# Kernel optimization log

Hardware: AMD Instinct MI355X
Metric: run time of the kernel (lower is better)

The kernel has to match this reference:

```python
import jax, jax.numpy as jnp
import numpy as np

N_NODES = 50000
N_EDGES = 800000
N_GRAPHS = 64
IN_DIM, HID, OUT = 128, 128, 16


def gcn_conv(x, src, dst, deg_inv_sqrt, W, b):
    # x: [N, Cin]; src/dst: [E+N] (self-loops appended); W: [Cin, Cout]
    h = x @ W                                   # [N, Cout]
    norm = deg_inv_sqrt[src] * deg_inv_sqrt[dst]  # [E+N]
    msg = h[src] * norm[:, None]                # gather + scale
    out = jax.ops.segment_sum(msg, dst, num_segments=N_NODES)
    return out + b


def setup_inputs() -> dict:
    key = jax.random.key(0)
    ks = jax.random.split(key, 8)
    x = jax.random.normal(ks[0], (N_NODES, IN_DIM), dtype=jnp.float32)
    edge_index = jax.random.randint(ks[1], (2, N_EDGES), 0, N_NODES, dtype=jnp.int64)
    batch = jnp.sort(jax.random.randint(ks[2], (N_NODES,), 0, N_GRAPHS, dtype=jnp.int64))
    s = 1.0 / np.sqrt(IN_DIM)
    W1 = jax.random.normal(ks[3], (IN_DIM, HID), dtype=jnp.float32) * s
    b1 = jnp.zeros((HID,), dtype=jnp.float32)
    W2 = jax.random.normal(ks[4], (HID, HID), dtype=jnp.float32) * (1.0 / np.sqrt(HID))
    b2 = jnp.zeros((HID,), dtype=jnp.float32)
    Wfc = jax.random.normal(ks[5], (HID, OUT), dtype=jnp.float32) * (1.0 / np.sqrt(HID))
    bfc = jnp.zeros((OUT,), dtype=jnp.float32)
    return {"x": x, "edge_index": edge_index, "batch": batch,
            "W1": W1, "b1": b1, "W2": W2, "b2": b2, "Wfc": Wfc, "bfc": bfc}


def reference(x, edge_index, batch, W1, b1, W2, b2, Wfc, bfc):
    self_loops = jnp.arange(N_NODES, dtype=edge_index.dtype)
    src = jnp.concatenate([edge_index[0], self_loops])  # [E+N]
    dst = jnp.concatenate([edge_index[1], self_loops])
    deg = jax.ops.segment_sum(jnp.ones_like(dst, dtype=x.dtype), dst, num_segments=N_NODES)
    deg_inv_sqrt = jnp.where(deg > 0, jax.lax.rsqrt(deg), 0.0)

    h = jax.nn.relu(gcn_conv(x, src, dst, deg_inv_sqrt, W1, b1))
    h = jax.nn.relu(gcn_conv(h, src, dst, deg_inv_sqrt, W2, b2))

    # global mean pool over graphs
    sums = jax.ops.segment_sum(h, batch, num_segments=N_GRAPHS)         # [G, HID]
    cnts = jax.ops.segment_sum(jnp.ones((N_NODES,), h.dtype), batch, num_segments=N_GRAPHS)
    pooled = sums / jnp.maximum(cnts, 1.0)[:, None]

    return pooled @ Wfc + bfc  # [G, OUT]
```

## Files before the change

kernel.cpp:

```cpp
#include <hip/hip_runtime.h>
#include <math.h>

#define N_NODES 50000
#define N_EDGES 800000
#define N_GRAPHS 64
#define DIM 128
#define OUTD 16

#define BSHIFT 8
#define BNODES 256
#define NBUCK ((N_NODES + BNODES - 1) / BNODES)
#define TILE 2048
#define RCAP 8192
#define BSLOT 4864
#define GEMMB 256
#define BIN_GRID ((N_EDGES + TILE - 1) / TILE)

typedef __attribute__((ext_vector_type(8))) short short8;
typedef __attribute__((ext_vector_type(4))) float f32x4;

static __device__ __forceinline__ unsigned short f2bf(float f) {
    unsigned u = __float_as_uint(f);
    u += 0x7fffu + ((u >> 16) & 1u);
    return (unsigned short)(u >> 16);
}
static __device__ __forceinline__ float bfl(unsigned u) {
    return __uint_as_float(u << 16);
}
static __device__ __forceinline__ float bfh(unsigned u) {
    return __uint_as_float(u & 0xffff0000u);
}

__global__ __launch_bounds__(256) void k_init(int* __restrict__ bcnt,
                                              float* __restrict__ pool,
                                              const float* __restrict__ W2,
                                              unsigned* __restrict__ W2f) {
    int tid = threadIdx.x;
    if (tid < NBUCK) bcnt[tid] = 0;
    for (int i = tid; i < N_GRAPHS * DIM; i += 256) pool[i] = 0.f;
    for (int idx = tid; idx < (DIM / 2) * DIM; idx += 256) {
        int kp = idx >> 7;
        int n  = idx & 127;
        int k  = kp * 2;
        int kstep = kp >> 4;
        int quad  = (kp >> 2) & 3;
        int jw    = kp & 3;
        int ct    = n >> 4;
        unsigned vlo = f2bf(W2[(size_t)k * DIM + n]);
        unsigned vhi = f2bf(W2[(size_t)(k + 1) * DIM + n]);
        W2f[(((kstep * 8 + ct) * 64) + quad * 16 + (n & 15)) * 4 + jw] = vlo | (vhi << 16);
    }
}

template <int BF16IN>
static __device__ __forceinline__ void gemm_body(const void* __restrict__ Av,
                                                 const float* __restrict__ Wg,
                                                 unsigned short* __restrict__ C,
                                                 int nrows,
                                                 unsigned* smemW, unsigned* smemC,
                                                 int tile0, int tstride) {
    unsigned* Wl = smemW;
    {
        int t = threadIdx.x;
        int p = t & 63;
        int kp = p * 2;
        int n0 = (t >> 6) * 32;
        int kstep = kp >> 5;
        int quad = (kp >> 3) & 3;
        int jw = (kp & 7) >> 1;
        const float* r0 = Wg + (size_t)kp * DIM;
        const float* r1 = r0 + DIM;
        int rot = (p >> 2) & 7;
#pragma unroll
        for (int i4 = 0; i4 < 8; ++i4) {
            int nb = ((i4 + rot) & 7) * 4;
            int n = n0 + nb;
            float4 lo = *(const float4*)(r0 + n);
            float4 hi = *(const float4*)(r1 + n);
            const float* lp = &lo.x;
            const float* hp = &hi.x;
#pragma unroll
            for (int ii = 0; ii < 4; ++ii) {
                int nn = n + ii;
                int ct = nn >> 4;
                int l  = quad * 16 + (nn & 15);
                unsigned vlo = f2bf(lp[ii]);
                unsigned vhi = f2bf(hp[ii]);
                Wl[(((kstep * 8 + ct) * 64) + l) * 4 + jw] = vlo | (vhi << 16);
            }
        }
    }
    __syncthreads();

    int wid  = threadIdx.x >> 6;
    int lane = threadIdx.x & 63;
    int m    = lane & 15;
    int quad = lane >> 4;
    const short8* Wf = (const short8*)Wl;
    unsigned short* cs = (unsigned short*)smemC + wid * 4352;
    const unsigned char* cb = (const unsigned char*)smemC + wid * 8704;

    int ntiles = (nrows + 127) / 128;
    for (int tile = tile0; tile < ntiles; tile += tstride) {
        int row0 = tile * 128 + wid * 32;
        if (row0 >= nrows) continue;

        int rA = row0 + m;      if (rA >= nrows) rA = nrows - 1;
        int rB = row0 + 16 + m; if (rB >= nrows) rB = nrows - 1;

        short8 af0[4], af1[4];
        if (BF16IN) {
            const unsigned short* arowA = (const unsigned short*)Av + (size_t)rA * DIM + quad * 8;
            const unsigned short* arowB = (const unsigned short*)Av + (size_t)rB * DIM + quad * 8;
#pragma unroll
            for (int ks = 0; ks < 4; ++ks) {
                af0[ks] = *(const short8*)(arowA + ks * 32);
                af1[ks] = *(const short8*)(arowB + ks * 32);
            }
        } else {
            const float* arowA = (const float*)Av + (size_t)rA * DIM + quad * 8;
            const float* arowB = (const float*)Av + (size_t)rB * DIM + quad * 8;
#pragma unroll
            for (int ks = 0; ks < 4; ++ks) {
                float4 lo = *(const float4*)(arowA + ks * 32);
                float4 hi = *(const float4*)(arowA + ks * 32 + 4);
                short8 f;
                f[0] = (short)f2bf(lo.x); f[1] = (short)f2bf(lo.y);
                f[2] = (short)f2bf(lo.z); f[3] = (short)f2bf(lo.w);
                f[4] = (short)f2bf(hi.x); f[5] = (short)f2bf(hi.y);
                f[6] = (short)f2bf(hi.z); f[7] = (short)f2bf(hi.w);
                af0[ks] = f;
                lo = *(const float4*)(arowB + ks * 32);
                hi = *(const float4*)(arowB + ks * 32 + 4);
                f[0] = (short)f2bf(lo.x); f[1] = (short)f2bf(lo.y);
                f[2] = (short)f2bf(lo.z); f[3] = (short)f2bf(lo.w);
                f[4] = (short)f2bf(hi.x); f[5] = (short)f2bf(hi.y);
                f[6] = (short)f2bf(hi.z); f[7] = (short)f2bf(hi.w);
                af1[ks] = f;
            }
        }

        f32x4 acc0[8], acc1[8];
#pragma unroll
        for (int ct = 0; ct < 8; ++ct) {
            acc0[ct] = (f32x4){0.f, 0.f, 0.f, 0.f};
            acc1[ct] = (f32x4){0.f, 0.f, 0.f, 0.f};
        }

#pragma unroll
        for (int ks = 0; ks < 4; ++ks) {
#pragma unroll
            for (int ct = 0; ct < 8; ++ct) {
                short8 bfrag = Wf[(ks * 8 + ct) * 64 + lane];
                acc0[ct] = __builtin_amdgcn_mfma_f32_16x16x32_bf16(af0[ks], bfrag, acc0[ct], 0, 0, 0);
                acc1[ct] = __builtin_amdgcn_mfma_f32_16x16x32_bf16(af1[ks], bfrag, acc1[ct], 0, 0, 0);
            }
        }

#pragma unroll
        for (int ct = 0; ct < 8; ++ct) {
#pragma unroll
            for (int reg = 0; reg < 4; ++reg) {
                cs[(quad * 4 + reg) * 136 + ct * 16 + m]      = f2bf(acc0[ct][reg]);
                cs[(16 + quad * 4 + reg) * 136 + ct * 16 + m] = f2bf(acc1[ct][reg]);
            }
        }
#pragma unroll
        for (int i = 0; i < 8; ++i) {
            int rg = i * 4 + quad;
            int r = row0 + rg;
            if (r < nrows) {
                uint4 vv = *(const uint4*)(cb + rg * 272 + m * 16);
                *((uint4*)(C + (size_t)r * DIM) + m) = vv;
            }
        }
    }
}

__global__ __launch_bounds__(256) void k_fused1(const float* __restrict__ A,
                                                const float* __restrict__ Wg,
                                                unsigned short* __restrict__ C,
                                                int nrows,
                                                const int* __restrict__ src,
                                                const int* __restrict__ dstp,
                                                int* __restrict__ bcnt,
                                                unsigned* __restrict__ bucket_arr) {
    __shared__ unsigned smemW[32768 / 4];
    __shared__ unsigned smemC[34816 / 4];
    if (blockIdx.x >= GEMMB) {
        int* cnt  = (int*)smemW;
        int* base = cnt + NBUCK;
        int tile0 = (blockIdx.x - GEMMB) * TILE;
        for (int i = threadIdx.x; i < NBUCK; i += 256) cnt[i] = 0;
        __syncthreads();
#pragma unroll
        for (int j = 0; j < TILE / 512; ++j) {
            int e = tile0 + j * 512 + threadIdx.x * 2;
            if (e < N_EDGES) {
                int2 d = *(const int2*)(dstp + e);
                atomicAdd(&cnt[d.x >> BSHIFT], 1);
                atomicAdd(&cnt[d.y >> BSHIFT], 1);
            }
        }
        __syncthreads();
        for (int i = threadIdx.x; i < NBUCK; i += 256) {
            int c = cnt[i];
            base[i] = i * BSLOT + (c ? atomicAdd(&bcnt[i], c) : 0);
            cnt[i] = 0;
        }
        __syncthreads();
#pragma unroll
        for (int j = 0; j < TILE / 512; ++j) {
            int e = tile0 + j * 512 + threadIdx.x * 2;
            if (e < N_EDGES) {
                int2 s = *(const int2*)(src + e);
                int2 d = *(const int2*)(dstp + e);
                int b0 = d.x >> BSHIFT, b1 = d.y >> BSHIFT;
                int p0 = base[b0] + atomicAdd(&cnt[b0], 1);
                bucket_arr[p0] = (unsigned)s.x | ((unsigned)(d.x & 255) << 16);
                int p1 = base[b1] + atomicAdd(&cnt[b1], 1);
                bucket_arr[p1] = (unsigned)s.y | ((unsigned)(d.y & 255) << 16);
            }
        }
        return;
    }
    gemm_body<0>(A, Wg, C, nrows, smemW, smemC, blockIdx.x, GEMMB);
}

__global__ __launch_bounds__(256) void k_binB(const unsigned* __restrict__ barr,
                                              const int* __restrict__ bcnt,
                                              int* __restrict__ row_off,
                                              float* __restrict__ dis,
                                              unsigned short* __restrict__ csr) {
    __shared__ unsigned raw[RCAP];
    __shared__ unsigned short stage[RCAP];
    __shared__ int hist[BNODES];
    __shared__ int scn[BNODES];
    __shared__ int borig[256], bscan[256];
    int tid = threadIdx.x;
    int b = blockIdx.x;
    int n0 = b << BSHIFT;

    int cv = (tid < NBUCK) ? bcnt[tid] : 0;
    borig[tid] = cv;
    bscan[tid] = cv;
    __syncthreads();
    for (int off = 1; off < 256; off <<= 1) {
        int t = (tid >= off) ? bscan[tid - off] : 0;
        __syncthreads();
        bscan[tid] += t;
        __syncthreads();
    }
    int rbase = bscan[b] - borig[b];
    int len = borig[b];
    const unsigned* bin = barr + (size_t)b * BSLOT;

    hist[tid] = 0;
    __syncthreads();
    for (int i = tid; i < len; i += 256) {
        unsigned ed = bin[i];
        if (i < RCAP) raw[i] = ed;
        atomicAdd(&hist[ed >> 16], 1);
    }
    __syncthreads();
    int v = hist[tid];
    scn[tid] = v;
    __syncthreads();
    for (int off = 1; off < 256; off <<= 1) {
        int t = (tid >= off) ? scn[tid - off] : 0;
        __syncthreads();
        scn[tid] += t;
        __syncthreads();
    }
    int excl = scn[tid] - v;
    int n = n0 + tid;
    if (n < N_NODES) {
        row_off[n] = rbase + excl;
        dis[n] = rsqrtf((float)(v + 1));
    }
    if (b == NBUCK - 1 && tid == 0) row_off[N_NODES] = N_EDGES;
    hist[tid] = excl;
    __syncthreads();
    for (int i = tid; i < len; i += 256) {
        unsigned ed = (i < RCAP) ? raw[i] : bin[i];
        int p = atomicAdd(&hist[ed >> 16], 1);
        unsigned short sv = (unsigned short)(ed & 0xffffu);
        if (p < RCAP) stage[p] = sv;
        else csr[rbase + p] = sv;
    }
    __syncthreads();
    {
        int s0 = excl, s1 = excl + v;
        for (int i = s0 + 1; i < s1; ++i) {
            unsigned short key = stage[i];
            int j = i - 1;
            while (j >= s0 && stage[j] > key) { stage[j + 1] = stage[j]; --j; }
            stage[j + 1] = key;
        }
    }
    __syncthreads();
    int lim = min(len, RCAP);
    for (int i = tid; i < lim; i += 256)
        csr[rbase + i] = stage[i];
}

template <int MODE>
__global__ __launch_bounds__(256) void k_agg(const uint4* __restrict__ Hb4,
                                             const int* __restrict__ row_off,
                                             const unsigned short* __restrict__ csr,
                                             const float* __restrict__ dis,
                                             const float* __restrict__ bias,
                                             uint4* __restrict__ out,
                                             const int* __restrict__ batch,
                                             float* __restrict__ pool,
                                             const short8* __restrict__ W2f) {
    __shared__ unsigned char smem[8768];
    int lane = threadIdx.x & 15;
    int nl   = threadIdx.x >> 4;
    int node = blockIdx.x * 16 + nl;

    float dn = dis[node];
    float wself = dn * dn;
    uint4 hp = Hb4[(size_t)node * 16 + lane];
    float a0[8], a1[8], a2[8], a3[8];
    a0[0] = wself * bfl(hp.x); a0[1] = wself * bfh(hp.x);
    a0[2] = wself * bfl(hp.y); a0[3] = wself * bfh(hp.y);
    a0[4] = wself * bfl(hp.z); a0[5] = wself * bfh(hp.z);
    a0[6] = wself * bfl(hp.w); a0[7] = wself * bfh(hp.w);
#pragma unroll
    for (int j = 0; j < 8; ++j) { a1[j] = 0.f; a2[j] = 0.f; a3[j] = 0.f; }

    int e = row_off[node], e1 = row_off[node + 1];
    for (; e + 4 <= e1; e += 4) {
        int s0 = csr[e];     int s1 = csr[e + 1];
        int s2 = csr[e + 2]; int s3 = csr[e + 3];
        uint4 g0 = Hb4[(size_t)s0 * 16 + lane];
        uint4 g1 = Hb4[(size_t)s1 * 16 + lane];
        uint4 g2 = Hb4[(size_t)s2 * 16 + lane];
        uint4 g3 = Hb4[(size_t)s3 * 16 + lane];
        float w0 = dn * dis[s0], w1 = dn * dis[s1];
        float w2 = dn * dis[s2], w3 = dn * dis[s3];
        a0[0] = fmaf(w0, bfl(g0.x), a0[0]); a0[1] = fmaf(w0, bfh(g0.x), a0[1]);
        a0[2] = fmaf(w0, bfl(g0.y), a0[2]); a0[3] = fmaf(w0, bfh(g0.y), a0[3]);
        a0[4] = fmaf(w0, bfl(g0.z), a0[4]); a0[5] = fmaf(w0, bfh(g0.z), a0[5]);
        a0[6] = fmaf(w0, bfl(g0.w), a0[6]); a0[7] = fmaf(w0, bfh(g0.w), a0[7]);
        a1[0] = fmaf(w1, bfl(g1.x), a1[0]); a1[1] = fmaf(w1, bfh(g1.x), a1[1]);
        a1[2] = fmaf(w1, bfl(g1.y), a1[2]); a1[3] = fmaf(w1, bfh(g1.y), a1[3]);
        a1[4] = fmaf(w1, bfl(g1.z), a1[4]); a1[5] = fmaf(w1, bfh(g1.z), a1[5]);
        a1[6] = fmaf(w1, bfl(g1.w), a1[6]); a1[7] = fmaf(w1, bfh(g1.w), a1[7]);
        a2[0] = fmaf(w2, bfl(g2.x), a2[0]); a2[1] = fmaf(w2, bfh(g2.x), a2[1]);
        a2[2] = fmaf(w2, bfl(g2.y), a2[2]); a2[3] = fmaf(w2, bfh(g2.y), a2[3]);
        a2[4] = fmaf(w2, bfl(g2.z), a2[4]); a2[5] = fmaf(w2, bfh(g2.z), a2[5]);
        a2[6] = fmaf(w2, bfl(g2.w), a2[6]); a2[7] = fmaf(w2, bfh(g2.w), a2[7]);
        a3[0] = fmaf(w3, bfl(g3.x), a3[0]); a3[1] = fmaf(w3, bfh(g3.x), a3[1]);
        a3[2] = fmaf(w3, bfl(g3.y), a3[2]); a3[3] = fmaf(w3, bfh(g3.y), a3[3]);
        a3[4] = fmaf(w3, bfl(g3.z), a3[4]); a3[5] = fmaf(w3, bfh(g3.z), a3[5]);
        a3[6] = fmaf(w3, bfl(g3.w), a3[6]); a3[7] = fmaf(w3, bfh(g3.w), a3[7]);
    }
    for (; e < e1; ++e) {
        int s = csr[e];
        uint4 g = Hb4[(size_t)s * 16 + lane];
        float w = dn * dis[s];
        a0[0] = fmaf(w, bfl(g.x), a0[0]); a0[1] = fmaf(w, bfh(g.x), a0[1]);
        a0[2] = fmaf(w, bfl(g.y), a0[2]); a0[3] = fmaf(w, bfh(g.y), a0[3]);
        a0[4] = fmaf(w, bfl(g.z), a0[4]); a0[5] = fmaf(w, bfh(g.z), a0[5]);
        a0[6] = fmaf(w, bfl(g.w), a0[6]); a0[7] = fmaf(w, bfh(g.w), a0[7]);
    }

    float4 b0 = ((const float4*)bias)[lane * 2];
    float4 b1v = ((const float4*)bias)[lane * 2 + 1];
    float r[8];
    r[0] = fmaxf(a0[0] + a1[0] + a2[0] + a3[0] + b0.x, 0.f);
    r[1] = fmaxf(a0[1] + a1[1] + a2[1] + a3[1] + b0.y, 0.f);
    r[2] = fmaxf(a0[2] + a1[2] + a2[2] + a3[2] + b0.z, 0.f);
    r[3] = fmaxf(a0[3] + a1[3] + a2[3] + a3[3] + b0.w, 0.f);
    r[4] = fmaxf(a0[4] + a1[4] + a2[4] + a3[4] + b1v.x, 0.f);
    r[5] = fmaxf(a0[5] + a1[5] + a2[5] + a3[5] + b1v.y, 0.f);
    r[6] = fmaxf(a0[6] + a1[6] + a2[6] + a3[6] + b1v.z, 0.f);
    r[7] = fmaxf(a0[7] + a1[7] + a2[7] + a3[7] + b1v.w, 0.f);

    if (MODE == 2) {
        unsigned short* sA = (unsigned short*)smem;
        unsigned short* sC = (unsigned short*)smem + 2176;
        uint4 av;
        av.x = (unsigned)f2bf(r[0]) | ((unsigned)f2bf(r[1]) << 16);
        av.y = (unsigned)f2bf(r[2]) | ((unsigned)f2bf(r[3]) << 16);
        av.z = (unsigned)f2bf(r[4]) | ((unsigned)f2bf(r[5]) << 16);
        av.w = (unsigned)f2bf(r[6]) | ((unsigned)f2bf(r[7]) << 16);
        *(uint4*)(sA + nl * 136 + lane * 8) = av;
        __syncthreads();

        int wid = threadIdx.x >> 6;
        int l64 = threadIdx.x & 63;
        int m   = l64 & 15;
        int q   = l64 >> 4;
        short8 af[4];
#pragma unroll
        for (int ks = 0; ks < 4; ++ks)
            af[ks] = *(const short8*)(sA + m * 136 + ks * 32 + q * 8);
        f32x4 acc[2];
        acc[0] = (f32x4){0.f, 0.f, 0.f, 0.f};
        acc[1] = (f32x4){0.f, 0.f, 0.f, 0.f};
#pragma unroll
        for (int ks = 0; ks < 4; ++ks) {
#pragma unroll
            for (int j = 0; j < 2; ++j) {
                int ct = wid * 2 + j;
                short8 bfrag = W2f[(ks * 8 + ct) * 64 + l64];
                acc[j] = __builtin_amdgcn_mfma_f32_16x16x32_bf16(af[ks], bfrag, acc[j], 0, 0, 0);
            }
        }
#pragma unroll
        for (int j = 0; j < 2; ++j) {
#pragma unroll
            for (int reg = 0; reg < 4; ++reg)
                sC[(q * 4 + reg) * 136 + (wid * 2 + j) * 16 + m] = f2bf(acc[j][reg]);
        }
        __syncthreads();
        {
            int t = threadIdx.x;
            int row = t >> 4, ch = t & 15;
            uint4 vv = *(const uint4*)((const unsigned char*)sC + row * 272 + ch * 16);
            out[(size_t)(blockIdx.x * 16 + row) * 16 + ch] = vv;
        }
    } else {
        float* sacc = (float*)smem;
        int* sg = (int*)(smem + 16 * DIM * 4);
#pragma unroll
        for (int j = 0; j < 8; ++j) sacc[nl * DIM + lane * 8 + j] = r[j];
        if (lane == 0) sg[nl] = batch[node];
        __syncthreads();
        int c = threadIdx.x;
        if (c < DIM) {
            float acc = 0.f;
            int curg = sg[0];
#pragma unroll
            for (int n2 = 0; n2 < 16; ++n2) {
                int g = sg[n2];
                if (g != curg) {
                    atomicAdd(&pool[curg * DIM + c], acc);
                    acc = 0.f; curg = g;
                }
                acc += sacc[n2 * DIM + c];
            }
            atomicAdd(&pool[curg * DIM + c], acc);
        }
    }
}

__global__ void k_fc(const float* __restrict__ pool, const int* __restrict__ batch,
                     const float* __restrict__ Wfc, const float* __restrict__ bfc,
                     float* __restrict__ out) {
    int id = blockIdx.x * blockDim.x + threadIdx.x;
    if (id >= N_GRAPHS * OUTD) return;
    int g = id >> 4, o = id & 15;
    int lo = 0, hi = N_NODES;
    while (lo < hi) { int mid = (lo + hi) >> 1; if (batch[mid] < g) lo = mid + 1; else hi = mid; }
    int l0 = lo;
    lo = 0; hi = N_NODES;
    while (lo < hi) { int mid = (lo + hi) >> 1; if (batch[mid] < g + 1) lo = mid + 1; else hi = mid; }
    int cntg = lo - l0;
    float inv = 1.0f / fmaxf((float)cntg, 1.0f);
    float acc = bfc[o];
    const float* p = pool + g * DIM;
    for (int c = 0; c < DIM; ++c)
        acc = fmaf(p[c] * inv, Wfc[c * OUTD + o], acc);
    out[id] = acc;
}


extern "C" void kernel_launch(void* const* d_in, const int* in_sizes, int n_in,
                              void* d_out, int out_size, void* d_ws, size_t ws_size,
                              hipStream_t stream) {
    const float* x    = (const float*)d_in[0];
    const int*   ei   = (const int*)d_in[1];
    const int*   batch= (const int*)d_in[2];
    const float* W1   = (const float*)d_in[3];
    const float* b1   = (const float*)d_in[4];
    const float* W2   = (const float*)d_in[5];
    const float* b2   = (const float*)d_in[6];
    const float* Wfc  = (const float*)d_in[7];
    const float* bfc  = (const float*)d_in[8];
    float* out = (float*)d_out;

    char* ws = (char*)d_ws;
    size_t off = 0;
    auto alloc = [&](size_t bytes) -> char* {
        char* p = ws + off;
        off = (off + bytes + 255) & ~(size_t)255;
        return p;
    };
    int*      bcnt     = (int*)     alloc((size_t)NBUCK * 4);
    int*      row_off  = (int*)     alloc((size_t)(N_NODES + 1) * 4);
    float*    dis      = (float*)   alloc((size_t)N_NODES * 4);
    unsigned short* csr= (unsigned short*)alloc((size_t)N_EDGES * 2);
    unsigned* barr     = (unsigned*)alloc((size_t)NBUCK * BSLOT * 4);
    float*    pool     = (float*)   alloc((size_t)N_GRAPHS * DIM * 4);
    unsigned* W2f      = (unsigned*)alloc((size_t)(DIM / 2) * DIM * 4);
    unsigned short* Hb = (unsigned short*)alloc((size_t)N_NODES * DIM * 2);
    unsigned short* Hb2= (unsigned short*)alloc((size_t)N_NODES * DIM * 2);

    const int* src = ei;
    const int* dst = ei + N_EDGES;

    k_init<<<1, 256, 0, stream>>>(bcnt, pool, W2, W2f);
    k_fused1<<<GEMMB + BIN_GRID, 256, 0, stream>>>(x, W1, Hb, N_NODES,
                                                   src, dst, bcnt, barr);
    k_binB<<<NBUCK, 256, 0, stream>>>(barr, bcnt, row_off, dis, csr);

    int agg_grid = (N_NODES + 15) / 16;
    k_agg<2><<<agg_grid, 256, 0, stream>>>((const uint4*)Hb, row_off, csr, dis, b1,
                                           (uint4*)Hb2, batch, pool, (const short8*)W2f);
    k_agg<1><<<agg_grid, 256, 0, stream>>>((const uint4*)Hb2, row_off, csr, dis, b2,
                                           nullptr, batch, pool, nullptr);
    k_fc<<<(N_GRAPHS * OUTD + 255) / 256, 256, 0, stream>>>(pool, batch, Wfc, bfc, out);
}
```

Before: 239.7 us.

## Prescale layer-2 features by source norm, drop CSR sort, fold init into binning

The second GCN layer's input is now pre-multiplied by its row's inverse-sqrt degree in the first aggregation's MFMA epilogue. The second aggregation can then sum gathered rows directly and apply the destination norm once, with no per-edge dis[] loads or multiplies. The per-row insertion sort of CSR neighbours is removed, which accepts an unsorted gather order and a nondeterministic float summation order. The separate k_init kernel is replaced by a memset plus block 0 of k_binB doing the pool zeroing and W2 conversion, saving one launch.

```diff
diff --git a/kernel.cpp b/kernel.cpp
--- a/kernel.cpp
+++ b/kernel.cpp
@@ -29,27 +29,6 @@
 }
 static __device__ __forceinline__ float bfh(unsigned u) {
     return __uint_as_float(u & 0xffff0000u);
-}
-
-__global__ __launch_bounds__(256) void k_init(int* __restrict__ bcnt,
-                                              float* __restrict__ pool,
-                                              const float* __restrict__ W2,
-                                              unsigned* __restrict__ W2f) {
-    int tid = threadIdx.x;
-    if (tid < NBUCK) bcnt[tid] = 0;
-    for (int i = tid; i < N_GRAPHS * DIM; i += 256) pool[i] = 0.f;
-    for (int idx = tid; idx < (DIM / 2) * DIM; idx += 256) {
-        int kp = idx >> 7;
-        int n  = idx & 127;
-        int k  = kp * 2;
-        int kstep = kp >> 4;
-        int quad  = (kp >> 2) & 3;
-        int jw    = kp & 3;
-        int ct    = n >> 4;
-        unsigned vlo = f2bf(W2[(size_t)k * DIM + n]);
-        unsigned vhi = f2bf(W2[(size_t)(k + 1) * DIM + n]);
-        W2f[(((kstep * 8 + ct) * 64) + quad * 16 + (n & 15)) * 4 + jw] = vlo | (vhi << 16);
-    }
 }
 
 template <int BF16IN>
@@ -231,7 +210,10 @@
                                               const int* __restrict__ bcnt,
                                               int* __restrict__ row_off,
                                               float* __restrict__ dis,
-                                              unsigned short* __restrict__ csr) {
+                                              unsigned short* __restrict__ csr,
+                                              const float* __restrict__ W2,
+                                              float* __restrict__ pool,
+                                              unsigned* __restrict__ W2f) {
     __shared__ unsigned raw[RCAP];
     __shared__ unsigned short stage[RCAP];
     __shared__ int hist[BNODES];
@@ -241,6 +223,22 @@
     int b = blockIdx.x;
     int n0 = b << BSHIFT;
 
+    if (b == 0) {
+        for (int i = tid; i < N_GRAPHS * DIM; i += 256) pool[i] = 0.f;
+        for (int idx = tid; idx < (DIM / 2) * DIM; idx += 256) {
+            int kp = idx >> 7;
+            int n  = idx & 127;
+            int k  = kp * 2;
+            int kstep = kp >> 4;
+            int quad  = (kp >> 2) & 3;
+            int jw    = kp & 3;
+            int ct    = n >> 4;
+            unsigned vlo = f2bf(W2[(size_t)k * DIM + n]);
+            unsigned vhi = f2bf(W2[(size_t)(k + 1) * DIM + n]);
+            W2f[(((kstep * 8 + ct) * 64) + quad * 16 + (n & 15)) * 4 + jw] = vlo | (vhi << 16);
+        }
+    }
+
     int cv = (tid < NBUCK) ? bcnt[tid] : 0;
     borig[tid] = cv;
     bscan[tid] = cv;
@@ -287,16 +285,6 @@
         unsigned short sv = (unsigned short)(ed & 0xffffu);
         if (p < RCAP) stage[p] = sv;
         else csr[rbase + p] = sv;
-    }
-    __syncthreads();
-    {
-        int s0 = excl, s1 = excl + v;
-        for (int i = s0 + 1; i < s1; ++i) {
-            unsigned short key = stage[i];
-            int j = i - 1;
-            while (j >= s0 && stage[j] > key) { stage[j + 1] = stage[j]; --j; }
-            stage[j + 1] = key;
-        }
     }
     __syncthreads();
     int lim = min(len, RCAP);
@@ -315,69 +303,113 @@
                                              float* __restrict__ pool,
                                              const short8* __restrict__ W2f) {
     __shared__ unsigned char smem[8768];
+    __shared__ float sdS[16];
     int lane = threadIdx.x & 15;
     int nl   = threadIdx.x >> 4;
     int node = blockIdx.x * 16 + nl;
 
     float dn = dis[node];
-    float wself = dn * dn;
+    if (lane == 0) sdS[nl] = dn;
     uint4 hp = Hb4[(size_t)node * 16 + lane];
     float a0[8], a1[8], a2[8], a3[8];
-    a0[0] = wself * bfl(hp.x); a0[1] = wself * bfh(hp.x);
-    a0[2] = wself * bfl(hp.y); a0[3] = wself * bfh(hp.y);
-    a0[4] = wself * bfl(hp.z); a0[5] = wself * bfh(hp.z);
-    a0[6] = wself * bfl(hp.w); a0[7] = wself * bfh(hp.w);
+    if (MODE == 2) {
+        float wself = dn * dn;
+        a0[0] = wself * bfl(hp.x); a0[1] = wself * bfh(hp.x);
+        a0[2] = wself * bfl(hp.y); a0[3] = wself * bfh(hp.y);
+        a0[4] = wself * bfl(hp.z); a0[5] = wself * bfh(hp.z);
+        a0[6] = wself * bfl(hp.w); a0[7] = wself * bfh(hp.w);
+    } else {
+        a0[0] = bfl(hp.x); a0[1] = bfh(hp.x);
+        a0[2] = bfl(hp.y); a0[3] = bfh(hp.y);
+        a0[4] = bfl(hp.z); a0[5] = bfh(hp.z);
+        a0[6] = bfl(hp.w); a0[7] = bfh(hp.w);
+    }
 #pragma unroll
     for (int j = 0; j < 8; ++j) { a1[j] = 0.f; a2[j] = 0.f; a3[j] = 0.f; }
 
     int e = row_off[node], e1 = row_off[node + 1];
-    for (; e + 4 <= e1; e += 4) {
-        int s0 = csr[e];     int s1 = csr[e + 1];
-        int s2 = csr[e + 2]; int s3 = csr[e + 3];
-        uint4 g0 = Hb4[(size_t)s0 * 16 + lane];
-        uint4 g1 = Hb4[(size_t)s1 * 16 + lane];
-        uint4 g2 = Hb4[(size_t)s2 * 16 + lane];
-        uint4 g3 = Hb4[(size_t)s3 * 16 + lane];
-        float w0 = dn * dis[s0], w1 = dn * dis[s1];
-        float w2 = dn * dis[s2], w3 = dn * dis[s3];
-        a0[0] = fmaf(w0, bfl(g0.x), a0[0]); a0[1] = fmaf(w0, bfh(g0.x), a0[1]);
-        a0[2] = fmaf(w0, bfl(g0.y), a0[2]); a0[3] = fmaf(w0, bfh(g0.y), a0[3]);
-        a0[4] = fmaf(w0, bfl(g0.z), a0[4]); a0[5] = fmaf(w0, bfh(g0.z), a0[5]);
-        a0[6] = fmaf(w0, bfl(g0.w), a0[6]); a0[7] = fmaf(w0, bfh(g0.w), a0[7]);
-        a1[0] = fmaf(w1, bfl(g1.x), a1[0]); a1[1] = fmaf(w1, bfh(g1.x), a1[1]);
-        a1[2] = fmaf(w1, bfl(g1.y), a1[2]); a1[3] = fmaf(w1, bfh(g1.y), a1[3]);
-        a1[4] = fmaf(w1, bfl(g1.z), a1[4]); a1[5] = fmaf(w1, bfh(g1.z), a1[5]);
-        a1[6] = fmaf(w1, bfl(g1.w), a1[6]); a1[7] = fmaf(w1, bfh(g1.w), a1[7]);
-        a2[0] = fmaf(w2, bfl(g2.x), a2[0]); a2[1] = fmaf(w2, bfh(g2.x), a2[1]);
-        a2[2] = fmaf(w2, bfl(g2.y), a2[2]); a2[3] = fmaf(w2, bfh(g2.y), a2[3]);
-        a2[4] = fmaf(w2, bfl(g2.z), a2[4]); a2[5] = fmaf(w2, bfh(g2.z), a2[5]);
-        a2[6] = fmaf(w2, bfl(g2.w), a2[6]); a2[7] = fmaf(w2, bfh(g2.w), a2[7]);
-        a3[0] = fmaf(w3, bfl(g3.x), a3[0]); a3[1] = fmaf(w3, bfh(g3.x), a3[1]);
-        a3[2] = fmaf(w3, bfl(g3.y), a3[2]); a3[3] = fmaf(w3, bfh(g3.y), a3[3]);
-        a3[4] = fmaf(w3, bfl(g3.z), a3[4]); a3[5] = fmaf(w3, bfh(g3.z), a3[5]);
-        a3[6] = fmaf(w3, bfl(g3.w), a3[6]); a3[7] = fmaf(w3, bfh(g3.w), a3[7]);
-    }
-    for (; e < e1; ++e) {
-        int s = csr[e];
-        uint4 g = Hb4[(size_t)s * 16 + lane];
-        float w = dn * dis[s];
-        a0[0] = fmaf(w, bfl(g.x), a0[0]); a0[1] = fmaf(w, bfh(g.x), a0[1]);
-        a0[2] = fmaf(w, bfl(g.y), a0[2]); a0[3] = fmaf(w, bfh(g.y), a0[3]);
-        a0[4] = fmaf(w, bfl(g.z), a0[4]); a0[5] = fmaf(w, bfh(g.z), a0[5]);
-        a0[6] = fmaf(w, bfl(g.w), a0[6]); a0[7] = fmaf(w, bfh(g.w), a0[7]);
+    if (MODE == 2) {
+        for (; e + 4 <= e1; e += 4) {
+            int s0 = csr[e];     int s1 = csr[e + 1];
+            int s2 = csr[e + 2]; int s3 = csr[e + 3];
+            uint4 g0 = Hb4[(size_t)s0 * 16 + lane];
+            uint4 g1 = Hb4[(size_t)s1 * 16 + lane];
+            uint4 g2 = Hb4[(size_t)s2 * 16 + lane];
+            uint4 g3 = Hb4[(size_t)s3 * 16 + lane];
+            float w0 = dn * dis[s0], w1 = dn * dis[s1];
+            float w2 = dn * dis[s2], w3 = dn * dis[s3];
+            a0[0] = fmaf(w0, bfl(g0.x), a0[0]); a0[1] = fmaf(w0, bfh(g0.x), a0[1]);
+            a0[2] = fmaf(w0, bfl(g0.y), a0[2]); a0[3] = fmaf(w0, bfh(g0.y), a0[3]);
+            a0[4] = fmaf(w0, bfl(g0.z), a0[4]); a0[5] = fmaf(w0, bfh(g0.z), a0[5]);
+            a0[6] = fmaf(w0, bfl(g0.w), a0[6]); a0[7] = fmaf(w0, bfh(g0.w), a0[7]);
+            a1[0] = fmaf(w1, bfl(g1.x), a1[0]); a1[1] = fmaf(w1, bfh(g1.x), a1[1]);
+            a1[2] = fmaf(w1, bfl(g1.y), a1[2]); a1[3] = fmaf(w1, bfh(g1.y), a1[3]);
+            a1[4] = fmaf(w1, bfl(g1.z), a1[4]); a1[5] = fmaf(w1, bfh(g1.z), a1[5]);
+            a1[6] = fmaf(w1, bfl(g1.w), a1[6]); a1[7] = fmaf(w1, bfh(g1.w), a1[7]);
+            a2[0] = fmaf(w2, bfl(g2.x), a2[0]); a2[1] = fmaf(w2, bfh(g2.x), a2[1]);
+            a2[2] = fmaf(w2, bfl(g2.y), a2[2]); a2[3] = fmaf(w2, bfh(g2.y), a2[3]);
+            a2[4] = fmaf(w2, bfl(g2.z), a2[4]); a2[5] = fmaf(w2, bfh(g2.z), a2[5]);
+            a2[6] = fmaf(w2, bfl(g2.w), a2[6]); a2[7] = fmaf(w2, bfh(g2.w), a2[7]);
+            a3[0] = fmaf(w3, bfl(g3.x), a3[0]); a3[1] = fmaf(w3, bfh(g3.x), a3[1]);
+            a3[2] = fmaf(w3, bfl(g3.y), a3[2]); a3[3] = fmaf(w3, bfh(g3.y), a3[3]);
+            a3[4] = fmaf(w3, bfl(g3.z), a3[4]); a3[5] = fmaf(w3, bfh(g3.z), a3[5]);
+            a3[6] = fmaf(w3, bfl(g3.w), a3[6]); a3[7] = fmaf(w3, bfh(g3.w), a3[7]);
+        }
+        for (; e < e1; ++e) {
+            int s = csr[e];
+            uint4 g = Hb4[(size_t)s * 16 + lane];
+            float w = dn * dis[s];
+            a0[0] = fmaf(w, bfl(g.x), a0[0]); a0[1] = fmaf(w, bfh(g.x), a0[1]);
+            a0[2] = fmaf(w, bfl(g.y), a0[2]); a0[3] = fmaf(w, bfh(g.y), a0[3]);
+            a0[4] = fmaf(w, bfl(g.z), a0[4]); a0[5] = fmaf(w, bfh(g.z), a0[5]);
+            a0[6] = fmaf(w, bfl(g.w), a0[6]); a0[7] = fmaf(w, bfh(g.w), a0[7]);
+        }
+    } else {
+#define ACC8(A, g) do { \
+        A[0] += bfl(g.x); A[1] += bfh(g.x); \
+        A[2] += bfl(g.y); A[3] += bfh(g.y); \
+        A[4] += bfl(g.z); A[5] += bfh(g.z); \
+        A[6] += bfl(g.w); A[7] += bfh(g.w); \
+    } while (0)
+        for (; e + 4 <= e1; e += 4) {
+            int s0 = csr[e];     int s1 = csr[e + 1];
+            int s2 = csr[e + 2]; int s3 = csr[e + 3];
+            uint4 g0 = Hb4[(size_t)s0 * 16 + lane];
+            uint4 g1 = Hb4[(size_t)s1 * 16 + lane];
+            uint4 g2 = Hb4[(size_t)s2 * 16 + lane];
+            uint4 g3 = Hb4[(size_t)s3 * 16 + lane];
+            ACC8(a0, g0); ACC8(a1, g1); ACC8(a2, g2); ACC8(a3, g3);
+        }
+        for (; e < e1; ++e) {
+            int s = csr[e];
+            uint4 g = Hb4[(size_t)s * 16 + lane];
+            ACC8(a0, g);
+        }
+#undef ACC8
     }
 
     float4 b0 = ((const float4*)bias)[lane * 2];
     float4 b1v = ((const float4*)bias)[lane * 2 + 1];
     float r[8];
-    r[0] = fmaxf(a0[0] + a1[0] + a2[0] + a3[0] + b0.x, 0.f);
-    r[1] = fmaxf(a0[1] + a1[1] + a2[1] + a3[1] + b0.y, 0.f);
-    r[2] = fmaxf(a0[2] + a1[2] + a2[2] + a3[2] + b0.z, 0.f);
-    r[3] = fmaxf(a0[3] + a1[3] + a2[3] + a3[3] + b0.w, 0.f);
-    r[4] = fmaxf(a0[4] + a1[4] + a2[4] + a3[4] + b1v.x, 0.f);
-    r[5] = fmaxf(a0[5] + a1[5] + a2[5] + a3[5] + b1v.y, 0.f);
-    r[6] = fmaxf(a0[6] + a1[6] + a2[6] + a3[6] + b1v.z, 0.f);
-    r[7] = fmaxf(a0[7] + a1[7] + a2[7] + a3[7] + b1v.w, 0.f);
+    if (MODE == 2) {
+        r[0] = fmaxf(a0[0] + a1[0] + a2[0] + a3[0] + b0.x, 0.f);
+        r[1] = fmaxf(a0[1] + a1[1] + a2[1] + a3[1] + b0.y, 0.f);
+        r[2] = fmaxf(a0[2] + a1[2] + a2[2] + a3[2] + b0.z, 0.f);
+        r[3] = fmaxf(a0[3] + a1[3] + a2[3] + a3[3] + b0.w, 0.f);
+        r[4] = fmaxf(a0[4] + a1[4] + a2[4] + a3[4] + b1v.x, 0.f);
+        r[5] = fmaxf(a0[5] + a1[5] + a2[5] + a3[5] + b1v.y, 0.f);
+        r[6] = fmaxf(a0[6] + a1[6] + a2[6] + a3[6] + b1v.z, 0.f);
+        r[7] = fmaxf(a0[7] + a1[7] + a2[7] + a3[7] + b1v.w, 0.f);
+    } else {
+        r[0] = fmaxf(fmaf(dn, a0[0] + a1[0] + a2[0] + a3[0], b0.x), 0.f);
+        r[1] = fmaxf(fmaf(dn, a0[1] + a1[1] + a2[1] + a3[1], b0.y), 0.f);
+        r[2] = fmaxf(fmaf(dn, a0[2] + a1[2] + a2[2] + a3[2], b0.z), 0.f);
+        r[3] = fmaxf(fmaf(dn, a0[3] + a1[3] + a2[3] + a3[3], b0.w), 0.f);
+        r[4] = fmaxf(fmaf(dn, a0[4] + a1[4] + a2[4] + a3[4], b1v.x), 0.f);
+        r[5] = fmaxf(fmaf(dn, a0[5] + a1[5] + a2[5] + a3[5], b1v.y), 0.f);
+        r[6] = fmaxf(fmaf(dn, a0[6] + a1[6] + a2[6] + a3[6], b1v.z), 0.f);
+        r[7] = fmaxf(fmaf(dn, a0[7] + a1[7] + a2[7] + a3[7], b1v.w), 0.f);
+    }
 
     if (MODE == 2) {
         unsigned short* sA = (unsigned short*)smem;
@@ -413,8 +445,10 @@
 #pragma unroll
         for (int j = 0; j < 2; ++j) {
 #pragma unroll
-            for (int reg = 0; reg < 4; ++reg)
-                sC[(q * 4 + reg) * 136 + (wid * 2 + j) * 16 + m] = f2bf(acc[j][reg]);
+            for (int reg = 0; reg < 4; ++reg) {
+                float sc = sdS[q * 4 + reg];
+                sC[(q * 4 + reg) * 136 + (wid * 2 + j) * 16 + m] = f2bf(acc[j][reg] * sc);
+            }
         }
         __syncthreads();
         {
@@ -503,10 +537,11 @@
     const int* src = ei;
     const int* dst = ei + N_EDGES;
 
-    k_init<<<1, 256, 0, stream>>>(bcnt, pool, W2, W2f);
+    hipMemsetAsync(bcnt, 0, (size_t)NBUCK * 4, stream);
     k_fused1<<<GEMMB + BIN_GRID, 256, 0, stream>>>(x, W1, Hb, N_NODES,
                                                    src, dst, bcnt, barr);
-    k_binB<<<NBUCK, 256, 0, stream>>>(barr, bcnt, row_off, dis, csr);
+    k_binB<<<NBUCK, 256, 0, stream>>>(barr, bcnt, row_off, dis, csr,
+                                      W2, pool, W2f);
 
     int agg_grid = (N_NODES + 15) / 16;
     k_agg<2><<<agg_grid, 256, 0, stream>>>((const uint4*)Hb, row_off, csr, dis, b1,
```

Result: faster. 202.4 us (-15.5%).
